# Optimization experiments

Measured on AMD Instinct MI355X. Metric: run time of the kernel, lower is better.

Reference implementation:

```python
import jax, jax.numpy as jnp
import numpy as np

SEED_THRESHOLD = 0.5
DUPLICATE_THRESHOLD = 0.8


def setup_inputs() -> dict:
    key = jax.random.key(0)
    k1, k2 = jax.random.split(key)
    B, Q, C = 16, 1800, 256
    return {
        "query_signatures": jax.random.normal(k1, (B, Q, C), dtype=jnp.float32),
        "query_seed_logits": jax.random.normal(k2, (B, Q), dtype=jnp.float32),
    }


def _cc_labels(adj):
    """Connected-component labels via min-label propagation. adj: [Q,Q] bool (symmetric).
    Label of each node = smallest node index in its component. Unconnected nodes keep own index."""
    Q = adj.shape[0]
    labels0 = jnp.arange(Q, dtype=jnp.int32)

    def cond(state):
        return state[1]

    def body(state):
        labels, _ = state
        nbr_min = jnp.min(jnp.where(adj, labels[None, :], Q), axis=1)
        new = jnp.minimum(labels, nbr_min)
        return new, jnp.any(new != labels)

    labels, _ = jax.lax.while_loop(cond, body, (labels0, jnp.bool_(True)))
    return labels


def reference(query_signatures, query_seed_logits):
    sig = query_signatures                     # [B,Q,C]
    B, Q, C = sig.shape
    qidx = jnp.arange(Q)

    scores = jax.nn.sigmoid(query_seed_logits.astype(jnp.float32))   # [B,Q]
    selected = scores >= SEED_THRESHOLD                               # [B,Q]
    # fallback: if no query selected in an image, select the argmax-score query
    empty = ~jnp.any(selected, axis=1)                                # [B]
    fb = jnp.argmax(scores, axis=1)                                   # [B]
    selected = selected | (empty[:, None] & (qidx[None, :] == fb[:, None]))

    # cosine pairwise similarity
    nrm = jnp.linalg.norm(sig, axis=-1, keepdims=True)
    nsig = sig / jnp.maximum(nrm, 1e-12)
    sim = jnp.einsum("bqc,bkc->bqk", nsig, nsig)                      # [B,Q,Q]

    adj = (sim >= DUPLICATE_THRESHOLD) & selected[:, :, None] & selected[:, None, :]
    adj = adj.at[:, qidx, qidx].set(selected)                         # diag = selected

    labels = jax.vmap(_cc_labels)(adj)                                # [B,Q] int32

    # a label slot l hosts a component iff node l is selected and is its own component min
    active = selected & (labels == qidx[None, :].astype(labels.dtype))  # [B,Q]

    # per-component best-score member (components visited in ascending min-index order,
    # matching the torch BFS-from-ascending-node order)
    member = (labels[:, None, :] == qidx[None, :, None].astype(labels.dtype)) & selected[:, None, :]  # [B,Ql,Qn]
    masked_scores = jnp.where(member, scores[:, None, :], -jnp.inf)
    best = jnp.argmax(masked_scores, axis=2)                          # [B,Q] node index of best per label
    best_sig = jnp.take_along_axis(sig, best[..., None], axis=1)      # [B,Q,C]
    best_score = jnp.take_along_axis(scores, best, axis=1)            # [B,Q]

    # compact active components to the front (pad to Q, the static max)
    pos = jnp.cumsum(active, axis=1) - 1
    dest = jnp.where(active, pos, Q)                                  # inactive -> dropped

    seed_signatures = jax.vmap(
        lambda d, v: jnp.zeros((Q, C), sig.dtype).at[d].set(v, mode="drop")
    )(dest, best_sig)
    seed_scores = jax.vmap(
        lambda d, v: jnp.zeros((Q,), scores.dtype).at[d].set(v, mode="drop")
    )(dest, best_score)

    num_seeds = jnp.sum(active, axis=1)
    pad_mask = qidx[None, :] < num_seeds[:, None]
    return seed_signatures, pad_mask, seed_scores
```

## Files before the change

### kernel.cpp

```cpp
#include <hip/hip_runtime.h>
#include <hip/hip_bf16.h>
#include <stdint.h>

#define B_ 16
#define Q_ 1800
#define C_ 256
#define WPR 29
#define QPAD 1856
#define TBK 15
#define NTRI 120
#define OUT_SIG_ELEMS (B_*Q_*C_)

typedef unsigned long long u64;
typedef unsigned int u32;
typedef __attribute__((ext_vector_type(8))) short bf16x8;
typedef __attribute__((ext_vector_type(4))) float f32x4;

__global__ __launch_bounds__(256)
void k_compact(const float* __restrict__ logits,
               int* __restrict__ sel_idx, int* __restrict__ sel_cnt) {
  int b = blockIdx.x, t = threadIdx.x;
  int lane = t & 63, wid = t >> 6;
  __shared__ int wsum[4];
  __shared__ int s_tot;
  __shared__ u64 kw[4];
  const float* lgb = logits + b * Q_;

  int f[8]; int cnt = 0;
  #pragma unroll
  for (int e = 0; e < 8; ++e) {
    int q = t * 8 + e; int fl = 0;
    if (q < Q_) fl = (lgb[q] >= 0.0f) ? 1 : 0;
    f[e] = fl; cnt += fl;
  }
  int incl = cnt;
  #pragma unroll
  for (int d = 1; d < 64; d <<= 1) {
    int v = __shfl_up(incl, d, 64);
    if (lane >= d) incl += v;
  }
  if (lane == 63) wsum[wid] = incl;
  __syncthreads();
  if (t == 0) {
    int acc = 0;
    #pragma unroll
    for (int i = 0; i < 4; ++i) { int v = wsum[i]; wsum[i] = acc; acc += v; }
    s_tot = acc;
  }
  __syncthreads();
  int excl = wsum[wid] + incl - cnt;
  int total = s_tot;

  if (total > 0) {
    #pragma unroll
    for (int e = 0; e < 8; ++e) {
      if (f[e]) { sel_idx[b * Q_ + excl] = t * 8 + e; excl++; }
    }
    if (t == 0) sel_cnt[b] = total;
  } else {
    u64 mk = 0;
    for (int q = t; q < Q_; q += 256) {
      float sc = 1.0f / (1.0f + expf(-lgb[q]));
      u64 key = ((u64)__float_as_uint(sc) << 32) | (u32)(~(u32)q);
      mk = (mk > key) ? mk : key;
    }
    #pragma unroll
    for (int d = 1; d < 64; d <<= 1) { u64 o = __shfl_xor(mk, d, 64); mk = (o > mk) ? o : mk; }
    if (lane == 0) kw[wid] = mk;
    __syncthreads();
    if (t == 0) {
      u64 m2 = kw[0];
      #pragma unroll
      for (int i = 1; i < 4; ++i) m2 = (kw[i] > m2) ? kw[i] : m2;
      sel_idx[b * Q_] = (int)(~(u32)m2);
      sel_cnt[b] = 1;
    }
  }
}

__global__ __launch_bounds__(256)
void k_prep(const float* __restrict__ sig, const int* __restrict__ sel_idx,
            const int* __restrict__ sel_cnt, unsigned short* __restrict__ nsig,
            u32* __restrict__ rowmin) {
  int b = blockIdx.y;
  int p = blockIdx.x * 4 + (threadIdx.x >> 6);
  int lane = threadIdx.x & 63;
  int S = sel_cnt[b];
  int Spad = (S + 63) & ~63;
  if (p >= Spad) return;
  if (lane == 0) rowmin[b * QPAD + p] = 0xFFFFFFFFu;
  unsigned short* dst = nsig + ((size_t)b * QPAD + p) * C_;
  if (p >= S) {
    *reinterpret_cast<uint2*>(dst + lane * 4) = make_uint2(0u, 0u);
    return;
  }
  int row = sel_idx[b * Q_ + p];
  const float* src = sig + ((size_t)b * Q_ + row) * C_;
  float4 v = *reinterpret_cast<const float4*>(src + lane * 4);
  float ss = v.x * v.x + v.y * v.y + v.z * v.z + v.w * v.w;
  #pragma unroll
  for (int m = 32; m; m >>= 1) ss += __shfl_xor(ss, m, 64);
  float inv = 1.0f / fmaxf(sqrtf(ss), 1e-12f);
  __hip_bfloat16 h0 = __float2bfloat16(v.x * inv);
  __hip_bfloat16 h1 = __float2bfloat16(v.y * inv);
  __hip_bfloat16 h2 = __float2bfloat16(v.z * inv);
  __hip_bfloat16 h3 = __float2bfloat16(v.w * inv);
  unsigned short u0, u1, u2, u3;
  __builtin_memcpy(&u0, &h0, 2); __builtin_memcpy(&u1, &h1, 2);
  __builtin_memcpy(&u2, &h2, 2); __builtin_memcpy(&u3, &h3, 2);
  uint2 wv;
  wv.x = (u32)u0 | ((u32)u1 << 16);
  wv.y = (u32)u2 | ((u32)u3 << 16);
  *reinterpret_cast<uint2*>(dst + lane * 4) = wv;
}

__global__ __launch_bounds__(256)
void k_sim(const unsigned short* __restrict__ nsig, const int* __restrict__ sel_cnt,
           u64* __restrict__ adj, u32* __restrict__ rowmin) {
  int lin = blockIdx.x;
  int b = lin & 15;
  int u = lin >> 4, tib = 0;
  while (u >= TBK - tib) { u -= TBK - tib; ++tib; }
  int tjb = tib + u;
  int S = sel_cnt[b];
  if (tjb * 128 >= S) return;
  const bool diag = (tib == tjb);

  __shared__ uint4 Alds[2048];
  __shared__ uint4 Blds[2048];
  __shared__ u64 adjtile[4][64];

  const int t = threadIdx.x;
  const int wv = t >> 6, lane = t & 63;
  const int lr = lane & 15, lg = lane >> 4;

  const int i1 = tib * 128 + (wv >> 1) * 64;
  const int j1 = tjb * 128 + (wv & 1) * 64;
  const bool live = (i1 < S) && (j1 < S);

  const char* gbase = (const char*)(nsig + (size_t)b * QPAD * C_);
  const char* arow = gbase + (size_t)tib * 128 * 512;
  const char* brow = gbase + (size_t)tjb * 128 * 512;

  f32x4 acc[4][4];
  #pragma unroll
  for (int rs = 0; rs < 4; ++rs)
    #pragma unroll
    for (int cg = 0; cg < 4; ++cg) acc[rs][cg] = (f32x4){0.f, 0.f, 0.f, 0.f};

  const int ra0 = (wv >> 1) * 64;
  const int rb0 = (wv & 1) * 64;
  const char* Bbase = reinterpret_cast<const char*>(diag ? Alds : Blds);

  for (int kh = 0; kh < 2; ++kh) {
    #pragma unroll
    for (int it = 0; it < 8; ++it) {
      int o = it * 4096 + t * 16;
      int r = o >> 8;
      int w = o & 255;
      int sw = o ^ ((r & 7) << 4);
      uint4 va = *reinterpret_cast<const uint4*>(arow + (size_t)r * 512 + kh * 256 + w);
      Alds[sw >> 4] = va;
      if (!diag) {
        uint4 vb = *reinterpret_cast<const uint4*>(brow + (size_t)r * 512 + kh * 256 + w);
        Blds[sw >> 4] = vb;
      }
    }
    __syncthreads();
    if (live) {
      #pragma unroll
      for (int ks = 0; ks < 4; ++ks) {
        bf16x8 af[4], bf[4];
        #pragma unroll
        for (int rs = 0; rs < 4; ++rs) {
          int r = ra0 + rs * 16 + lr;
          int byte = r * 256 + ((ks * 64 + lg * 16) ^ ((r & 7) << 4));
          af[rs] = *reinterpret_cast<const bf16x8*>(
              reinterpret_cast<const char*>(Alds) + byte);
        }
        #pragma unroll
        for (int cg = 0; cg < 4; ++cg) {
          int r = rb0 + cg * 16 + lr;
          int byte = r * 256 + ((ks * 64 + lg * 16) ^ ((r & 7) << 4));
          bf[cg] = *reinterpret_cast<const bf16x8*>(Bbase + byte);
        }
        #pragma unroll
        for (int rs = 0; rs < 4; ++rs)
          #pragma unroll
          for (int cg = 0; cg < 4; ++cg)
            acc[rs][cg] = __builtin_amdgcn_mfma_f32_16x16x32_bf16(
                af[rs], bf[cg], acc[rs][cg], 0, 0, 0);
      }
    }
    __syncthreads();
  }

  if (!live) return;
  adjtile[wv][lane] = 0ull;
  #pragma unroll
  for (int rs = 0; rs < 4; ++rs) {
    #pragma unroll
    for (int j = 0; j < 4; ++j) {
      u64 bits = 0ull;
      if (acc[rs][0][j] >= 0.8f) bits |= 1ull << (0  + lr);
      if (acc[rs][1][j] >= 0.8f) bits |= 1ull << (16 + lr);
      if (acc[rs][2][j] >= 0.8f) bits |= 1ull << (32 + lr);
      if (acc[rs][3][j] >= 0.8f) bits |= 1ull << (48 + lr);
      if (bits) atomicOr(&adjtile[wv][rs * 16 + lg * 4 + j], bits);
    }
  }
  int gi = i1 + lane;
  u64 word = adjtile[wv][lane];
  if (gi < S) {
    adj[((size_t)b * Q_ + gi) * WPR + (j1 >> 6)] = word;
    if (word) atomicMin(&rowmin[b * QPAD + gi], (u32)(j1 + __builtin_ctzll(word)));
  }
  if (!diag) {
    u64 tw = 0ull;
    for (int i = 0; i < 64; ++i)
      tw |= ((adjtile[wv][i] >> lane) & 1ull) << i;
    int gj = j1 + lane;
    if (gj < S) {
      adj[((size_t)b * Q_ + gj) * WPR + (i1 >> 6)] = tw;
      if (tw) atomicMin(&rowmin[b * QPAD + gj], (u32)(i1 + __builtin_ctzll(tw)));
    }
  }
}

__global__ __launch_bounds__(256)
void k_ccgather(const float* __restrict__ sig, const float* __restrict__ logits,
                const int* __restrict__ sel_idx, const int* __restrict__ sel_cnt,
                const u64* __restrict__ adj, const u32* __restrict__ rowmin,
                float* __restrict__ out_sig, float* __restrict__ out_mask,
                float* __restrict__ out_scores) {
  const int b = blockIdx.y, g = blockIdx.x;
  const int t = threadIdx.x, lane = t & 63, wid = t >> 6;
  __shared__ int lab[Q_];
  __shared__ int lab2[Q_];
  __shared__ u64 best[Q_];
  __shared__ int wsum[4];
  __shared__ int s_tot;
  __shared__ int s_dirty;

  const int S = sel_cnt[b];
  if (t == 0) s_dirty = 0;
  __syncthreads();
  for (int s = t; s < S; s += 256)
    if (rowmin[b * QPAD + s] != (u32)s) s_dirty = 1;
  __syncthreads();

  const int p = g * 4 + wid;
  float* orow = out_sig + ((size_t)b * Q_ + p) * C_;

  if (!s_dirty) {
    if (p < S) {
      int row = sel_idx[b * Q_ + p];
      float4 v = *reinterpret_cast<const float4*>(sig + ((size_t)b * Q_ + row) * C_ + lane * 4);
      *reinterpret_cast<float4*>(orow + lane * 4) = v;
      if (lane == 0) {
        out_mask[b * Q_ + p] = 1.0f;
        out_scores[b * Q_ + p] = 1.0f / (1.0f + expf(-logits[b * Q_ + row]));
      }
    } else {
      *reinterpret_cast<float4*>(orow + lane * 4) = make_float4(0.f, 0.f, 0.f, 0.f);
      if (lane == 0) {
        out_mask[b * Q_ + p] = 0.0f;
        out_scores[b * Q_ + p] = 0.0f;
      }
    }
    return;
  }

  const int nw = (S + 63) >> 6;
  const u64* arow0 = adj + (size_t)b * Q_ * WPR;
  __shared__ int s_chg;

  if (t == 0) s_chg = 1;
  for (int s = t; s < S; s += 256) {
    u32 m = rowmin[b * QPAD + s];
    lab[s] = (int)(((u32)s < m) ? (u32)s : m);
  }
  __syncthreads();
  for (int iter = 0; iter < Q_ + 2; ++iter) {
    if (t == 0) s_chg = 0;
    __syncthreads();
    for (int s = t; s < S; s += 256) {
      int m = lab[s];
      const u64* row = arow0 + (size_t)s * WPR;
      for (int w = 0; w < nw; ++w) {
        u64 msk = row[w];
        while (msk) {
          int j = (w << 6) + __builtin_ctzll(msk);
          int lj = lab[j];
          m = (lj < m) ? lj : m;
          msk &= msk - 1;
        }
      }
      lab2[s] = m;
      if (m != lab[s]) s_chg = 1;
    }
    __syncthreads();
    int ch = s_chg;
    for (int s = t; s < S; s += 256) lab[s] = lab2[s];
    __syncthreads();
    if (!ch) break;
  }

  for (int s = t; s < S; s += 256) best[s] = 0ull;
  __syncthreads();
  const int* sidx = sel_idx + b * Q_;
  for (int s = t; s < S; s += 256) {
    int orig = sidx[s];
    float sc = 1.0f / (1.0f + expf(-logits[b * Q_ + orig]));
    u64 key = ((u64)__float_as_uint(sc) << 32) | (u32)(~(u32)orig);
    atomicMax(&best[lab[s]], key);
  }
  __syncthreads();

  __shared__ int slot[4];
  int rf[8]; int rcnt = 0;
  #pragma unroll
  for (int e = 0; e < 8; ++e) {
    int s = t * 8 + e;
    int fl = (s < S && lab[s] == s) ? 1 : 0;
    rf[e] = fl; rcnt += fl;
  }
  int rincl = rcnt;
  #pragma unroll
  for (int d = 1; d < 64; d <<= 1) {
    int v = __shfl_up(rincl, d, 64);
    if (lane >= d) rincl += v;
  }
  if (t < 4) slot[t] = -1;
  if (lane == 63) wsum[wid] = rincl;
  __syncthreads();
  if (t == 0) {
    int acc = 0;
    #pragma unroll
    for (int i = 0; i < 4; ++i) { int v = wsum[i]; wsum[i] = acc; acc += v; }
    s_tot = acc;
  }
  __syncthreads();
  int rex = wsum[wid] + rincl - rcnt;
  #pragma unroll
  for (int e = 0; e < 8; ++e) {
    if (rf[e]) {
      if (rex >= g * 4 && rex < g * 4 + 4) slot[rex - g * 4] = t * 8 + e;
      rex++;
    }
  }
  __syncthreads();
  int n = s_tot;

  if (p < n) {
    u64 key = best[slot[wid]];
    int orig = (int)(~(u32)key);
    float4 v = *reinterpret_cast<const float4*>(sig + ((size_t)b * Q_ + orig) * C_ + lane * 4);
    *reinterpret_cast<float4*>(orow + lane * 4) = v;
    if (lane == 0) {
      out_mask[b * Q_ + p] = 1.0f;
      out_scores[b * Q_ + p] = __uint_as_float((u32)(key >> 32));
    }
  } else {
    *reinterpret_cast<float4*>(orow + lane * 4) = make_float4(0.f, 0.f, 0.f, 0.f);
    if (lane == 0) {
      out_mask[b * Q_ + p] = 0.0f;
      out_scores[b * Q_ + p] = 0.0f;
    }
  }
}

__global__ __launch_bounds__(1024)
void k_cc2(const float* __restrict__ logits, const int* __restrict__ sel_idx,
           const int* __restrict__ sel_cnt, const u64* __restrict__ adj,
           const u32* __restrict__ rowmin,
           int* __restrict__ best_idx, float* __restrict__ best_sc,
           int* __restrict__ nroots) {
  int b = blockIdx.x, t = threadIdx.x;
  int lane = t & 63, wid = t >> 6;
  __shared__ int lab[Q_];
  __shared__ int lab2[Q_];
  __shared__ u64 best[Q_];
  __shared__ int wsum[16];
  __shared__ int s_tot;
  __shared__ int s_changed;

  int S = sel_cnt[b];
  int nw = (S + 63) >> 6;
  const u64* arow0 = adj + (size_t)b * Q_ * WPR;

  if (t == 0) s_changed = 0;
  __syncthreads();
  for (int s = t; s < S; s += 1024) {
    u32 m = rowmin[b * QPAD + s];
    u32 v = ((u32)s < m) ? (u32)s : m;
    lab[s] = (int)v;
    if (v != (u32)s) s_changed = 1;
  }
  __syncthreads();

  if (s_changed) {
    for (int iter = 0; iter < Q_ + 2; ++iter) {
      if (t == 0) s_changed = 0;
      __syncthreads();
      for (int s = t; s < S; s += 1024) {
        int m = lab[s];
        const u64* row = arow0 + (size_t)s * WPR;
        for (int w = 0; w < nw; ++w) {
          u64 msk = row[w];
          while (msk) {
            int j = (w << 6) + __builtin_ctzll(msk);
            int lj = lab[j];
            m = (lj < m) ? lj : m;
            msk &= msk - 1;
          }
        }
        lab2[s] = m;
        if (m != lab[s]) s_changed = 1;
      }
      __syncthreads();
      int ch = s_changed;
      for (int s = t; s < S; s += 1024) lab[s] = lab2[s];
      __syncthreads();
      if (!ch) break;
    }
  }

  for (int s = t; s < S; s += 1024) best[s] = 0ull;
  __syncthreads();
  const int* sidx = sel_idx + b * Q_;
  for (int s = t; s < S; s += 1024) {
    int orig = sidx[s];
    float sc = 1.0f / (1.0f + expf(-logits[b * Q_ + orig]));
    u64 key = ((u64)__float_as_uint(sc) << 32) | (u32)(~(u32)orig);
    atomicMax(&best[lab[s]], key);
  }
  __syncthreads();

  int f[2]; int cnt = 0;
  #pragma unroll
  for (int e = 0; e < 2; ++e) {
    int s = t * 2 + e;
    int fl = (s < S && lab[s] == s) ? 1 : 0;
    f[e] = fl; cnt += fl;
  }
  int incl = cnt;
  #pragma unroll
  for (int d = 1; d < 64; d <<= 1) {
    int v = __shfl_up(incl, d, 64);
    if (lane >= d) incl += v;
  }
  if (lane == 63) wsum[wid] = incl;
  __syncthreads();
  if (t == 0) {
    int acc = 0;
    #pragma unroll
    for (int i = 0; i < 16; ++i) { int v = wsum[i]; wsum[i] = acc; acc += v; }
    s_tot = acc;
  }
  __syncthreads();
  int excl = wsum[wid] + incl - cnt;
  #pragma unroll
  for (int e = 0; e < 2; ++e) {
    if (f[e]) {
      int s = t * 2 + e;
      u64 key = best[s];
      best_idx[b * Q_ + excl] = (int)(~(u32)key);
      best_sc[b * Q_ + excl] = __uint_as_float((u32)(key >> 32));
      excl++;
    }
  }
  if (t == 0) nroots[b] = s_tot;
}

__global__ __launch_bounds__(256)
void k_gather(const float* __restrict__ sig, const int* __restrict__ best_idx,
              const float* __restrict__ best_sc, const int* __restrict__ nroots,
              float* __restrict__ out_sig, float* __restrict__ out_mask,
              float* __restrict__ out_scores) {
  int b = blockIdx.y;
  int p = blockIdx.x * 4 + (threadIdx.x >> 6);
  int lane = threadIdx.x & 63;
  if (p >= Q_) return;
  int n = nroots[b];
  float* orow = out_sig + ((size_t)b * Q_ + p) * C_;
  if (p < n) {
    int row = best_idx[b * Q_ + p];
    float4 v = *reinterpret_cast<const float4*>(sig + ((size_t)b * Q_ + row) * C_ + lane * 4);
    *reinterpret_cast<float4*>(orow + lane * 4) = v;
    if (lane == 0) {
      out_mask[b * Q_ + p] = 1.0f;
      out_scores[b * Q_ + p] = best_sc[b * Q_ + p];
    }
  } else {
    *reinterpret_cast<float4*>(orow + lane * 4) = make_float4(0.f, 0.f, 0.f, 0.f);
    if (lane == 0) {
      out_mask[b * Q_ + p] = 0.0f;
      out_scores[b * Q_ + p] = 0.0f;
    }
  }
}

extern "C" void kernel_launch(void* const* d_in, const int* in_sizes, int n_in,
                              void* d_out, int out_size, void* d_ws, size_t ws_size,
                              hipStream_t stream) {
  const float* p0 = (const float*)d_in[0];
  const float* p1 = (const float*)d_in[1];
  const float* sig;  const float* logits;
  if (in_sizes[0] == B_ * Q_ * C_) { sig = p0; logits = p1; }
  else                             { sig = p1; logits = p0; }

  float* out = (float*)d_out;
  float* out_mask   = out + OUT_SIG_ELEMS;
  float* out_scores = out + OUT_SIG_ELEMS + B_ * Q_;

  unsigned short* nsig = (unsigned short*)((char*)d_out + (size_t)(8u << 20));

  char* w = (char*)d_ws;
  int* sel_cnt = (int*)w;  w += 256;
  int* sel_idx = (int*)w;  w += B_ * Q_ * 4;

  const size_t need_big = 256 + (size_t)B_ * Q_ * 4 +
                          (size_t)B_ * QPAD * 4 + (size_t)B_ * Q_ * WPR * 8;
  dim3 gp(QPAD / 4, B_);
  dim3 gg(Q_ / 4, B_);

  if (ws_size >= need_big) {
    u32* rowmin = (u32*)w;  w += (size_t)B_ * QPAD * 4;
    u64* adj    = (u64*)w;

    k_compact<<<B_, 256, 0, stream>>>(logits, sel_idx, sel_cnt);
    k_prep<<<gp, 256, 0, stream>>>(sig, sel_idx, sel_cnt, nsig, rowmin);
    k_sim<<<B_ * NTRI, 256, 0, stream>>>(nsig, sel_cnt, adj, rowmin);
    k_ccgather<<<gg, 256, 0, stream>>>(sig, logits, sel_idx, sel_cnt, adj, rowmin,
                                       out, out_mask, out_scores);
  } else {
    int* best_idx  = (int*)w;   w += B_ * Q_ * 4;
    float* best_sc = (float*)w; w += B_ * Q_ * 4;
    int* nroots    = (int*)w;   w += 256;
    u64* adj    = (u64*)d_out;
    u32* rowmin = (u32*)((char*)d_out + (size_t)(26u << 20));

    k_compact<<<B_, 256, 0, stream>>>(logits, sel_idx, sel_cnt);
    k_prep<<<gp, 256, 0, stream>>>(sig, sel_idx, sel_cnt, nsig, rowmin);
    k_sim<<<B_ * NTRI, 256, 0, stream>>>(nsig, sel_cnt, adj, rowmin);
    k_cc2<<<B_, 1024, 0, stream>>>(logits, sel_idx, sel_cnt, adj, rowmin,
                                   best_idx, best_sc, nroots);
    k_gather<<<gg, 256, 0, stream>>>(sig, best_idx, best_sc, nroots,
                                     out, out_mask, out_scores);
  }
}
```

Baseline: 46.76 us.

## Write speculative singleton outputs in prep and repair only batches with duplicates

The prep kernel now also writes the output assuming every selected query is its own component: the sig row, the mask, and the sigmoid score. The similarity kernel sets a per-batch dirty flag when any off-diagonal adjacency bit appears. A new per-batch fix kernel reruns the label propagation, best-member selection and gather only for dirty batches, replacing the separate ccgather pass in the main path. For random inputs duplicates are rare, so the full connected-components and gather pass is mostly skipped. The cost is a larger workspace, and a dirty batch is written twice by a single 1024-thread block.

```diff
diff --git a/kernel.cpp b/kernel.cpp
--- a/kernel.cpp
+++ b/kernel.cpp
@@ -18,13 +18,15 @@
 
 __global__ __launch_bounds__(256)
 void k_compact(const float* __restrict__ logits,
-               int* __restrict__ sel_idx, int* __restrict__ sel_cnt) {
+               int* __restrict__ sel_idx, int* __restrict__ sel_cnt,
+               int* __restrict__ dirty) {
   int b = blockIdx.x, t = threadIdx.x;
   int lane = t & 63, wid = t >> 6;
   __shared__ int wsum[4];
   __shared__ int s_tot;
   __shared__ u64 kw[4];
   const float* lgb = logits + b * Q_;
+  if (t == 0) dirty[b] = 0;
 
   int f[8]; int cnt = 0;
   #pragma unroll
@@ -74,6 +76,62 @@
       for (int i = 1; i < 4; ++i) m2 = (kw[i] > m2) ? kw[i] : m2;
       sel_idx[b * Q_] = (int)(~(u32)m2);
       sel_cnt[b] = 1;
+    }
+  }
+}
+
+__global__ __launch_bounds__(256)
+void k_prepg(const float* __restrict__ sig, const float* __restrict__ logits,
+             const int* __restrict__ sel_idx, const int* __restrict__ sel_cnt,
+             unsigned short* __restrict__ nsig, u32* __restrict__ rowmin,
+             float* __restrict__ out_sig, float* __restrict__ out_mask,
+             float* __restrict__ out_scores) {
+  int b = blockIdx.y;
+  int p = blockIdx.x * 4 + (threadIdx.x >> 6);
+  int lane = threadIdx.x & 63;
+  int S = sel_cnt[b];
+  int Spad = (S + 63) & ~63;
+
+  if (p < Spad && lane == 0) rowmin[b * QPAD + p] = 0xFFFFFFFFu;
+
+  if (p < S) {
+    int row = sel_idx[b * Q_ + p];
+    const float* src = sig + ((size_t)b * Q_ + row) * C_;
+    float4 v = *reinterpret_cast<const float4*>(src + lane * 4);
+
+    float* orow = out_sig + ((size_t)b * Q_ + p) * C_;
+    *reinterpret_cast<float4*>(orow + lane * 4) = v;
+    if (lane == 0) {
+      out_mask[b * Q_ + p] = 1.0f;
+      out_scores[b * Q_ + p] = 1.0f / (1.0f + expf(-logits[b * Q_ + row]));
+    }
+
+    float ss = v.x * v.x + v.y * v.y + v.z * v.z + v.w * v.w;
+    #pragma unroll
+    for (int m = 32; m; m >>= 1) ss += __shfl_xor(ss, m, 64);
+    float inv = 1.0f / fmaxf(sqrtf(ss), 1e-12f);
+    __hip_bfloat16 h0 = __float2bfloat16(v.x * inv);
+    __hip_bfloat16 h1 = __float2bfloat16(v.y * inv);
+    __hip_bfloat16 h2 = __float2bfloat16(v.z * inv);
+    __hip_bfloat16 h3 = __float2bfloat16(v.w * inv);
+    unsigned short u0, u1, u2, u3;
+    __builtin_memcpy(&u0, &h0, 2); __builtin_memcpy(&u1, &h1, 2);
+    __builtin_memcpy(&u2, &h2, 2); __builtin_memcpy(&u3, &h3, 2);
+    uint2 wv;
+    wv.x = (u32)u0 | ((u32)u1 << 16);
+    wv.y = (u32)u2 | ((u32)u3 << 16);
+    *reinterpret_cast<uint2*>(nsig + ((size_t)b * QPAD + p) * C_ + lane * 4) = wv;
+  } else {
+    if (p < Spad)
+      *reinterpret_cast<uint2*>(nsig + ((size_t)b * QPAD + p) * C_ + lane * 4) =
+          make_uint2(0u, 0u);
+    if (p < Q_) {
+      float* orow = out_sig + ((size_t)b * Q_ + p) * C_;
+      *reinterpret_cast<float4*>(orow + lane * 4) = make_float4(0.f, 0.f, 0.f, 0.f);
+      if (lane == 0) {
+        out_mask[b * Q_ + p] = 0.0f;
+        out_scores[b * Q_ + p] = 0.0f;
+      }
     }
   }
 }
@@ -116,7 +174,8 @@
 
 __global__ __launch_bounds__(256)
 void k_sim(const unsigned short* __restrict__ nsig, const int* __restrict__ sel_cnt,
-           u64* __restrict__ adj, u32* __restrict__ rowmin) {
+           u64* __restrict__ adj, u32* __restrict__ rowmin,
+           int* __restrict__ dirty) {
   int lin = blockIdx.x;
   int b = lin & 15;
   int u = lin >> 4, tib = 0;
@@ -211,6 +270,9 @@
   }
   int gi = i1 + lane;
   u64 word = adjtile[wv][lane];
+  u64 selfbit = (i1 == j1) ? (1ull << lane) : 0ull;
+  bool offd = (gi < S) && ((word & ~selfbit) != 0ull);
+  if (__any(offd) && lane == 0) atomicOr(&dirty[b], 1);
   if (gi < S) {
     adj[((size_t)b * Q_ + gi) * WPR + (j1 >> 6)] = word;
     if (word) atomicMin(&rowmin[b * QPAD + gi], (u32)(j1 + __builtin_ctzll(word)));
@@ -223,6 +285,126 @@
     if (gj < S) {
       adj[((size_t)b * Q_ + gj) * WPR + (i1 >> 6)] = tw;
       if (tw) atomicMin(&rowmin[b * QPAD + gj], (u32)(i1 + __builtin_ctzll(tw)));
+    }
+  }
+}
+
+__global__ __launch_bounds__(1024)
+void k_fix(const float* __restrict__ sig, const float* __restrict__ logits,
+           const int* __restrict__ sel_idx, const int* __restrict__ sel_cnt,
+           const u64* __restrict__ adj, const u32* __restrict__ rowmin,
+           const int* __restrict__ dirty,
+           int* __restrict__ best_idx, float* __restrict__ best_sc,
+           float* __restrict__ out_sig, float* __restrict__ out_mask,
+           float* __restrict__ out_scores) {
+  int b = blockIdx.x;
+  if (!dirty[b]) return;
+  int t = threadIdx.x;
+  int lane = t & 63, wid = t >> 6;
+  __shared__ int lab[Q_];
+  __shared__ int lab2[Q_];
+  __shared__ u64 best[Q_];
+  __shared__ int wsum[16];
+  __shared__ int s_tot;
+  __shared__ int s_changed;
+
+  int S = sel_cnt[b];
+  int nw = (S + 63) >> 6;
+  const u64* arow0 = adj + (size_t)b * Q_ * WPR;
+
+  for (int s = t; s < S; s += 1024) {
+    u32 m = rowmin[b * QPAD + s];
+    lab[s] = (int)(((u32)s < m) ? (u32)s : m);
+  }
+  __syncthreads();
+  for (int iter = 0; iter < Q_ + 2; ++iter) {
+    if (t == 0) s_changed = 0;
+    __syncthreads();
+    for (int s = t; s < S; s += 1024) {
+      int m = lab[s];
+      const u64* row = arow0 + (size_t)s * WPR;
+      for (int w = 0; w < nw; ++w) {
+        u64 msk = row[w];
+        while (msk) {
+          int j = (w << 6) + __builtin_ctzll(msk);
+          int lj = lab[j];
+          m = (lj < m) ? lj : m;
+          msk &= msk - 1;
+        }
+      }
+      lab2[s] = m;
+      if (m != lab[s]) s_changed = 1;
+    }
+    __syncthreads();
+    int ch = s_changed;
+    for (int s = t; s < S; s += 1024) lab[s] = lab2[s];
+    __syncthreads();
+    if (!ch) break;
+  }
+
+  for (int s = t; s < S; s += 1024) best[s] = 0ull;
+  __syncthreads();
+  const int* sidx = sel_idx + b * Q_;
+  for (int s = t; s < S; s += 1024) {
+    int orig = sidx[s];
+    float sc = 1.0f / (1.0f + expf(-logits[b * Q_ + orig]));
+    u64 key = ((u64)__float_as_uint(sc) << 32) | (u32)(~(u32)orig);
+    atomicMax(&best[lab[s]], key);
+  }
+  __syncthreads();
+
+  int f[2]; int cnt = 0;
+  #pragma unroll
+  for (int e = 0; e < 2; ++e) {
+    int s = t * 2 + e;
+    int fl = (s < S && lab[s] == s) ? 1 : 0;
+    f[e] = fl; cnt += fl;
+  }
+  int incl = cnt;
+  #pragma unroll
+  for (int d = 1; d < 64; d <<= 1) {
+    int v = __shfl_up(incl, d, 64);
+    if (lane >= d) incl += v;
+  }
+  if (lane == 63) wsum[wid] = incl;
+  __syncthreads();
+  if (t == 0) {
+    int acc = 0;
+    #pragma unroll
+    for (int i = 0; i < 16; ++i) { int v = wsum[i]; wsum[i] = acc; acc += v; }
+    s_tot = acc;
+  }
+  __syncthreads();
+  int excl = wsum[wid] + incl - cnt;
+  #pragma unroll
+  for (int e = 0; e < 2; ++e) {
+    if (f[e]) {
+      int s = t * 2 + e;
+      u64 key = best[s];
+      best_idx[b * Q_ + excl] = (int)(~(u32)key);
+      best_sc[b * Q_ + excl] = __uint_as_float((u32)(key >> 32));
+      excl++;
+    }
+  }
+  __syncthreads();
+  int n = s_tot;
+
+  for (int p = wid; p < Q_; p += 16) {
+    float* orow = out_sig + ((size_t)b * Q_ + p) * C_;
+    if (p < n) {
+      int row = best_idx[b * Q_ + p];
+      float4 v = *reinterpret_cast<const float4*>(sig + ((size_t)b * Q_ + row) * C_ + lane * 4);
+      *reinterpret_cast<float4*>(orow + lane * 4) = v;
+      if (lane == 0) {
+        out_mask[b * Q_ + p] = 1.0f;
+        out_scores[b * Q_ + p] = best_sc[b * Q_ + p];
+      }
+    } else {
+      *reinterpret_cast<float4*>(orow + lane * 4) = make_float4(0.f, 0.f, 0.f, 0.f);
+      if (lane == 0) {
+        out_mask[b * Q_ + p] = 0.0f;
+        out_scores[b * Q_ + p] = 0.0f;
+      }
     }
   }
 }
@@ -370,137 +552,6 @@
   }
 }
 
-__global__ __launch_bounds__(1024)
-void k_cc2(const float* __restrict__ logits, const int* __restrict__ sel_idx,
-           const int* __restrict__ sel_cnt, const u64* __restrict__ adj,
-           const u32* __restrict__ rowmin,
-           int* __restrict__ best_idx, float* __restrict__ best_sc,
-           int* __restrict__ nroots) {
-  int b = blockIdx.x, t = threadIdx.x;
-  int lane = t & 63, wid = t >> 6;
-  __shared__ int lab[Q_];
-  __shared__ int lab2[Q_];
-  __shared__ u64 best[Q_];
-  __shared__ int wsum[16];
-  __shared__ int s_tot;
-  __shared__ int s_changed;
-
-  int S = sel_cnt[b];
-  int nw = (S + 63) >> 6;
-  const u64* arow0 = adj + (size_t)b * Q_ * WPR;
-
-  if (t == 0) s_changed = 0;
-  __syncthreads();
-  for (int s = t; s < S; s += 1024) {
-    u32 m = rowmin[b * QPAD + s];
-    u32 v = ((u32)s < m) ? (u32)s : m;
-    lab[s] = (int)v;
-    if (v != (u32)s) s_changed = 1;
-  }
-  __syncthreads();
-
-  if (s_changed) {
-    for (int iter = 0; iter < Q_ + 2; ++iter) {
-      if (t == 0) s_changed = 0;
-      __syncthreads();
-      for (int s = t; s < S; s += 1024) {
-        int m = lab[s];
-        const u64* row = arow0 + (size_t)s * WPR;
-        for (int w = 0; w < nw; ++w) {
-          u64 msk = row[w];
-          while (msk) {
-            int j = (w << 6) + __builtin_ctzll(msk);
-            int lj = lab[j];
-            m = (lj < m) ? lj : m;
-            msk &= msk - 1;
-          }
-        }
-        lab2[s] = m;
-        if (m != lab[s]) s_changed = 1;
-      }
-      __syncthreads();
-      int ch = s_changed;
-      for (int s = t; s < S; s += 1024) lab[s] = lab2[s];
-      __syncthreads();
-      if (!ch) break;
-    }
-  }
-
-  for (int s = t; s < S; s += 1024) best[s] = 0ull;
-  __syncthreads();
-  const int* sidx = sel_idx + b * Q_;
-  for (int s = t; s < S; s += 1024) {
-    int orig = sidx[s];
-    float sc = 1.0f / (1.0f + expf(-logits[b * Q_ + orig]));
-    u64 key = ((u64)__float_as_uint(sc) << 32) | (u32)(~(u32)orig);
-    atomicMax(&best[lab[s]], key);
-  }
-  __syncthreads();
-
-  int f[2]; int cnt = 0;
-  #pragma unroll
-  for (int e = 0; e < 2; ++e) {
-    int s = t * 2 + e;
-    int fl = (s < S && lab[s] == s) ? 1 : 0;
-    f[e] = fl; cnt += fl;
-  }
-  int incl = cnt;
-  #pragma unroll
-  for (int d = 1; d < 64; d <<= 1) {
-    int v = __shfl_up(incl, d, 64);
-    if (lane >= d) incl += v;
-  }
-  if (lane == 63) wsum[wid] = incl;
-  __syncthreads();
-  if (t == 0) {
-    int acc = 0;
-    #pragma unroll
-    for (int i = 0; i < 16; ++i) { int v = wsum[i]; wsum[i] = acc; acc += v; }
-    s_tot = acc;
-  }
-  __syncthreads();
-  int excl = wsum[wid] + incl - cnt;
-  #pragma unroll
-  for (int e = 0; e < 2; ++e) {
-    if (f[e]) {
-      int s = t * 2 + e;
-      u64 key = best[s];
-      best_idx[b * Q_ + excl] = (int)(~(u32)key);
-      best_sc[b * Q_ + excl] = __uint_as_float((u32)(key >> 32));
-      excl++;
-    }
-  }
-  if (t == 0) nroots[b] = s_tot;
-}
-
-__global__ __launch_bounds__(256)
-void k_gather(const float* __restrict__ sig, const int* __restrict__ best_idx,
-              const float* __restrict__ best_sc, const int* __restrict__ nroots,
-              float* __restrict__ out_sig, float* __restrict__ out_mask,
-              float* __restrict__ out_scores) {
-  int b = blockIdx.y;
-  int p = blockIdx.x * 4 + (threadIdx.x >> 6);
-  int lane = threadIdx.x & 63;
-  if (p >= Q_) return;
-  int n = nroots[b];
-  float* orow = out_sig + ((size_t)b * Q_ + p) * C_;
-  if (p < n) {
-    int row = best_idx[b * Q_ + p];
-    float4 v = *reinterpret_cast<const float4*>(sig + ((size_t)b * Q_ + row) * C_ + lane * 4);
-    *reinterpret_cast<float4*>(orow + lane * 4) = v;
-    if (lane == 0) {
-      out_mask[b * Q_ + p] = 1.0f;
-      out_scores[b * Q_ + p] = best_sc[b * Q_ + p];
-    }
-  } else {
-    *reinterpret_cast<float4*>(orow + lane * 4) = make_float4(0.f, 0.f, 0.f, 0.f);
-    if (lane == 0) {
-      out_mask[b * Q_ + p] = 0.0f;
-      out_scores[b * Q_ + p] = 0.0f;
-    }
-  }
-}
-
 extern "C" void kernel_launch(void* const* d_in, const int* in_sizes, int n_in,
                               void* d_out, int out_size, void* d_ws, size_t ws_size,
                               hipStream_t stream) {
@@ -514,39 +565,54 @@
   float* out_mask   = out + OUT_SIG_ELEMS;
   float* out_scores = out + OUT_SIG_ELEMS + B_ * Q_;
 
-  unsigned short* nsig = (unsigned short*)((char*)d_out + (size_t)(8u << 20));
-
   char* w = (char*)d_ws;
   int* sel_cnt = (int*)w;  w += 256;
+  int* dirty   = (int*)w;  w += 256;
   int* sel_idx = (int*)w;  w += B_ * Q_ * 4;
 
-  const size_t need_big = 256 + (size_t)B_ * Q_ * 4 +
-                          (size_t)B_ * QPAD * 4 + (size_t)B_ * Q_ * WPR * 8;
   dim3 gp(QPAD / 4, B_);
   dim3 gg(Q_ / 4, B_);
 
-  if (ws_size >= need_big) {
+  const size_t need_A = 512 + 3 * (size_t)B_ * Q_ * 4 + (size_t)B_ * QPAD * 4 +
+                        (size_t)B_ * Q_ * WPR * 8 + (size_t)B_ * QPAD * C_ * 2;
+  const size_t need_B = 512 + (size_t)B_ * Q_ * 4 + (size_t)B_ * QPAD * 4 +
+                        (size_t)B_ * Q_ * WPR * 8;
+
+  if (ws_size >= need_A) {
+    int* best_idx  = (int*)w;   w += B_ * Q_ * 4;
+    float* best_sc = (float*)w; w += B_ * Q_ * 4;
+    u32* rowmin = (u32*)w;      w += (size_t)B_ * QPAD * 4;
+    u64* adj    = (u64*)w;      w += (size_t)B_ * Q_ * WPR * 8;
+    unsigned short* nsig = (unsigned short*)w;
+
+    k_compact<<<B_, 256, 0, stream>>>(logits, sel_idx, sel_cnt, dirty);
+    k_prepg<<<gp, 256, 0, stream>>>(sig, logits, sel_idx, sel_cnt, nsig, rowmin,
+                                    out, out_mask, out_scores);
+    k_sim<<<B_ * NTRI, 256, 0, stream>>>(nsig, sel_cnt, adj, rowmin, dirty);
+    k_fix<<<B_, 1024, 0, stream>>>(sig, logits, sel_idx, sel_cnt, adj, rowmin,
+                                   dirty, best_idx, best_sc,
+                                   out, out_mask, out_scores);
+  } else if (ws_size >= need_B) {
     u32* rowmin = (u32*)w;  w += (size_t)B_ * QPAD * 4;
     u64* adj    = (u64*)w;
-
-    k_compact<<<B_, 256, 0, stream>>>(logits, sel_idx, sel_cnt);
+    unsigned short* nsig = (unsigned short*)((char*)d_out + (size_t)(8u << 20));
+
+    k_compact<<<B_, 256, 0, stream>>>(logits, sel_idx, sel_cnt, dirty);
     k_prep<<<gp, 256, 0, stream>>>(sig, sel_idx, sel_cnt, nsig, rowmin);
-    k_sim<<<B_ * NTRI, 256, 0, stream>>>(nsig, sel_cnt, adj, rowmin);
+    k_sim<<<B_ * NTRI, 256, 0, stream>>>(nsig, sel_cnt, adj, rowmin, dirty);
     k_ccgather<<<gg, 256, 0, stream>>>(sig, logits, sel_idx, sel_cnt, adj, rowmin,
                                        out, out_mask, out_scores);
   } else {
-    int* best_idx  = (int*)w;   w += B_ * Q_ * 4;
-    float* best_sc = (float*)w; w += B_ * Q_ * 4;
-    int* nroots    = (int*)w;   w += 256;
     u64* adj    = (u64*)d_out;
     u32* rowmin = (u32*)((char*)d_out + (size_t)(26u << 20));
-
-    k_compact<<<B_, 256, 0, stream>>>(logits, sel_idx, sel_cnt);
+    unsigned short* nsig = (unsigned short*)((char*)d_out + (size_t)(8u << 20));
+    int* best_idx  = (int*)w;   w += B_ * Q_ * 4;
+    float* best_sc = (float*)w;
+
+    k_compact<<<B_, 256, 0, stream>>>(logits, sel_idx, sel_cnt, dirty);
     k_prep<<<gp, 256, 0, stream>>>(sig, sel_idx, sel_cnt, nsig, rowmin);
-    k_sim<<<B_ * NTRI, 256, 0, stream>>>(nsig, sel_cnt, adj, rowmin);
-    k_cc2<<<B_, 1024, 0, stream>>>(logits, sel_idx, sel_cnt, adj, rowmin,
-                                   best_idx, best_sc, nroots);
-    k_gather<<<gg, 256, 0, stream>>>(sig, best_idx, best_sc, nroots,
-                                     out, out_mask, out_scores);
+    k_sim<<<B_ * NTRI, 256, 0, stream>>>(nsig, sel_cnt, adj, rowmin, dirty);
+    k_ccgather<<<gg, 256, 0, stream>>>(sig, logits, sel_idx, sel_cnt, adj, rowmin,
+                                       out, out_mask, out_scores);
   }
 }
```

After: 39.54 us. 15.4% less time.
